# Kernel optimization log

Measured on AMD Instinct MI355X. Metric: run time of the kernel, lower is better.

Reference implementation:

```python
import jax, jax.numpy as jnp
import numpy as np

N = 100000   # nodes
E = 800000   # directed edges
IN = 256     # in_channels (== hidden, required by repo's vn MLP dims)
HID = 256    # hidden_channels
OUT = 40     # out_channels (arxiv classes)
EPS = 1e-5


def setup_inputs() -> dict:
    key = jax.random.key(0)
    ks = jax.random.split(key, 8)
    def nrm(k, shape, scale=0.05):
        return jax.random.normal(k, shape, dtype=jnp.float32) * scale
    return {
        "x": nrm(ks[0], (N, IN), 1.0),
        "edge_index": jax.random.randint(ks[1], (2, E), 0, N, dtype=jnp.int32),
        # GCNConv weights (PyG: x @ W, then normalized aggregation, then + bias)
        "W0": nrm(ks[2], (IN, HID)),  "b0": jnp.zeros((HID,), jnp.float32),
        "W1": nrm(ks[3], (HID, HID)), "b1": jnp.zeros((HID,), jnp.float32),
        "W2": nrm(ks[4], (HID, OUT)), "b2": jnp.zeros((OUT,), jnp.float32),
        # BatchNorm1d affine params (batch-stat math, training mode)
        "bn_g0": jnp.ones((HID,), jnp.float32), "bn_b0": jnp.zeros((HID,), jnp.float32),
        "bn_g1": jnp.ones((HID,), jnp.float32), "bn_b1": jnp.zeros((HID,), jnp.float32),
        # virtual node embedding (init to 0 per reset_parameters)
        "vn_emb": jnp.zeros((1, IN), jnp.float32),
        # mlp_vns[0]: Linear(IN,HID) + LayerNorm(HID) + ReLU
        "vn_W0": nrm(ks[5], (IN, HID)),  "vn_b0": jnp.zeros((HID,), jnp.float32),
        "ln_g0": jnp.ones((HID,), jnp.float32), "ln_b0": jnp.zeros((HID,), jnp.float32),
        # mlp_vns[1]: Linear(HID,HID) + LayerNorm(HID) + ReLU
        "vn_W1": nrm(ks[6], (HID, HID)), "vn_b1": jnp.zeros((HID,), jnp.float32),
        "ln_g1": jnp.ones((HID,), jnp.float32), "ln_b1": jnp.zeros((HID,), jnp.float32),
    }


def _forward(x, edge_index, W0, b0, W1, b1, W2, b2, bn_g0, bn_b0, bn_g1, bn_b1,
             vn_emb, vn_W0, vn_b0, ln_g0, ln_b0, vn_W1, vn_b1, ln_g1, ln_b1):
    src, dst = edge_index[0], edge_index[1]
    # GCN symmetric normalization with self-loops: deg = in-degree + 1
    deg = jax.ops.segment_sum(jnp.ones(src.shape, jnp.float32), dst, num_segments=N) + 1.0
    dis = jax.lax.rsqrt(deg)                       # deg^{-1/2}  [N]
    coef = (dis[src] * dis[dst])[:, None]          # edge norm   [E,1]
    self_coef = (dis * dis)[:, None]               # self-loop norm = deg^{-1}  [N,1]

    def gcn(h, W, b):
        h = h @ W                                             # [N, out]
        agg = jax.ops.segment_sum(h[src] * coef, dst, num_segments=N)
        return agg + h * self_coef + b

    def bn(h, g, bv):  # BatchNorm1d, batch statistics over nodes
        mu = h.mean(0)
        var = ((h - mu) ** 2).mean(0)
        return (h - mu) * jax.lax.rsqrt(var + EPS) * g + bv

    def ln(h, g, bv):  # LayerNorm over last dim
        mu = h.mean(-1, keepdims=True)
        var = ((h - mu) ** 2).mean(-1, keepdims=True)
        return (h - mu) * jax.lax.rsqrt(var + EPS) * g + bv

    vx = vn_emb                                   # [1, IN]
    # layer 0
    h = x + vx                                    # virtual-node broadcast
    h = gcn(h, W0, b0)
    h = jax.nn.relu(bn(h, bn_g0, bn_b0))          # dropout = identity (eval)
    pool = jnp.sum(h, axis=0, keepdims=True)      # global_add_pool
    vx = jax.nn.relu(ln((pool + vx) @ vn_W0 + vn_b0, ln_g0, ln_b0))
    # layer 1
    h = h + vx
    h = gcn(h, W1, b1)
    h = jax.nn.relu(bn(h, bn_g1, bn_b1))
    pool = jnp.sum(h, axis=0, keepdims=True)
    vx = jax.nn.relu(ln((pool + vx) @ vn_W1 + vn_b1, ln_g1, ln_b1))
    # layer 2 (output)
    h = h + vx
    h = gcn(h, W2, b2)
    return jax.nn.log_softmax(h, axis=-1)


def reference(x, edge_index, W0, b0, W1, b1, W2, b2, bn_g0, bn_b0, bn_g1, bn_b1,
              vn_emb, vn_W0, vn_b0, ln_g0, ln_b0, vn_W1, vn_b1, ln_g1, ln_b1):
    return _forward(x, edge_index, W0, b0, W1, b1, W2, b2, bn_g0, bn_b0, bn_g1, bn_b1,
                    vn_emb, vn_W0, vn_b0, ln_g0, ln_b0, vn_W1, vn_b1, ln_g1, ln_b1)
```

## Files before the change

kernel.cpp:

```cpp
#include <hip/hip_runtime.h>
#include <hip/hip_bf16.h>
#include <cstdint>

#define N_NODES 100000
#define N_EDGES 800000
#define CH      256
#define COUT    40
#define COUTP   48
#define EPS     1e-5f
#define SCAN_CHUNK 1024
#define NSCAN_BLK  98
#define AGG_NPW 16
#define AGG_BLOCKS 2048
#define AGG_WAVES  (AGG_BLOCKS * 4)

typedef unsigned short u16;
typedef unsigned int   u32;
typedef short s16x8 __attribute__((ext_vector_type(8)));
typedef float f32x4 __attribute__((ext_vector_type(4)));

__device__ __forceinline__ float b2f(u32 u) { return __uint_as_float(u << 16); }
__device__ __forceinline__ u16 f2b(float f) {
    u32 u = __float_as_uint(f);
    u32 r = (u + 0x7fffu + ((u >> 16) & 1u)) >> 16;
    return (u16)r;
}
__device__ __forceinline__ u32 packb(float a, float b) {
    return (u32)f2b(a) | ((u32)f2b(b) << 16);
}
__device__ __forceinline__ void unpack8(uint4 v, float* f) {
    f[0] = b2f(v.x & 0xffffu); f[1] = b2f(v.x >> 16);
    f[2] = b2f(v.y & 0xffffu); f[3] = b2f(v.y >> 16);
    f[4] = b2f(v.z & 0xffffu); f[5] = b2f(v.z >> 16);
    f[6] = b2f(v.w & 0xffffu); f[7] = b2f(v.w >> 16);
}

__global__ void k_count(const int* __restrict__ dst, int* __restrict__ counts) {
    int e = blockIdx.x * 256 + threadIdx.x;
    if (e < N_EDGES) atomicAdd(&counts[dst[e]], 1);
}

__global__ void k_scan1(const int* __restrict__ counts, int* __restrict__ partial,
                        int* __restrict__ blocksums) {
    __shared__ int sdata[256];
    int base = blockIdx.x * SCAN_CHUNK;
    int t = threadIdx.x;
    int v[4]; int s = 0;
    for (int j = 0; j < 4; j++) {
        int i = base + t * 4 + j;
        v[j] = (i < N_NODES) ? counts[i] : 0;
        s += v[j];
    }
    sdata[t] = s; __syncthreads();
    for (int off = 1; off < 256; off <<= 1) {
        int x = (t >= off) ? sdata[t - off] : 0;
        __syncthreads();
        sdata[t] += x;
        __syncthreads();
    }
    int incl = sdata[t];
    int run = incl - s;
    if (t == 255) blocksums[blockIdx.x] = incl;
    for (int j = 0; j < 4; j++) {
        int i = base + t * 4 + j;
        if (i < N_NODES) partial[i] = run;
        run += v[j];
    }
}

__global__ void k_scan2(int* __restrict__ blocksums) {
    __shared__ int sd[128];
    int t = threadIdx.x;
    int v = (t < NSCAN_BLK) ? blocksums[t] : 0;
    sd[t] = v; __syncthreads();
    for (int off = 1; off < 128; off <<= 1) {
        int x = (t >= off) ? sd[t - off] : 0;
        __syncthreads();
        sd[t] += x;
        __syncthreads();
    }
    if (t < NSCAN_BLK) blocksums[t] = sd[t] - v;
}

__global__ void k_scan3(int* __restrict__ row_start, const int* __restrict__ blocksums,
                        int* __restrict__ cursor, const int* __restrict__ counts,
                        float* __restrict__ dis) {
    int i = blockIdx.x * 256 + threadIdx.x;
    if (i < N_NODES) {
        int v = row_start[i] + blocksums[i >> 10];
        row_start[i] = v;
        cursor[i] = v;
        dis[i] = rsqrtf(1.0f + (float)counts[i]);
    }
}

__global__ void k_fill(const int* __restrict__ src, const int* __restrict__ dst,
                       int* __restrict__ cursor, int2* __restrict__ edata,
                       const float* __restrict__ dis) {
    int e = blockIdx.x * 256 + threadIdx.x;
    if (e < N_EDGES) {
        int d = dst[e], s = src[e];
        int p = atomicAdd(&cursor[d], 1);
        int2 v; v.x = s; v.y = __float_as_int(dis[s] * dis[d]);
        edata[p] = v;
    }
}

__global__ void k_wt3(const float* __restrict__ W0, const float* __restrict__ W1,
                      const float* __restrict__ W2,
                      u16* __restrict__ T0, u16* __restrict__ T1, u16* __restrict__ T2) {
    int b = blockIdx.x, k = threadIdx.x;
    if (b < 256) {
        T0[b * 256 + k] = f2b(W0[k * 256 + b]);
    } else if (b < 512) {
        int n = b - 256;
        T1[n * 256 + k] = f2b(W1[k * 256 + n]);
    } else {
        int n = b - 512;
        T2[n * 256 + k] = f2b(n < COUT ? W2[k * COUT + n] : 0.f);
    }
}

__global__ void k_vecmat(const float* __restrict__ vec, const float* __restrict__ W,
                         int ncols, int npad, float* __restrict__ outv) {
    __shared__ float s[256];
    int t = threadIdx.x;
    s[t] = vec[t];
    __syncthreads();
    float acc = 0.f;
    if (t < ncols) {
        for (int k = 0; k < 256; k++) acc += s[k] * W[k * ncols + t];
    }
    if (t < npad) outv[t] = acc;
}

__global__ __launch_bounds__(256) void k_gemm_f32a(const float* __restrict__ A,
                                                   const u16* __restrict__ Wt,
                                                   u16* __restrict__ Hout) {
    __shared__ u16 Bs[256 * 72];
    __shared__ u16 As[64 * 72];
    const int t = threadIdx.x;
    const int wave = t >> 6, lane = t & 63;
    const int lm = lane & 15, quad = lane >> 4;
    const int m0 = blockIdx.x * 64;
    const int ar = t >> 2, as_ = (t & 3) * 16;
    const int arow = m0 + ar;
    const f32x4 vz = {0.f, 0.f, 0.f, 0.f};
    f32x4 acc[4][4];
    for (int m = 0; m < 4; m++)
        for (int c = 0; c < 4; c++) acc[m][c] = vz;

    for (int k0 = 0; k0 < 256; k0 += 64) {
        {
            const uint4* bsrc = (const uint4*)(Wt + t * 256 + k0);
            uint4* bdst = (uint4*)(Bs + t * 72);
#pragma unroll
            for (int j = 0; j < 8; j++) bdst[j] = bsrc[j];
            uint4 p0 = {0,0,0,0}, p1 = {0,0,0,0};
            if (arow < N_NODES) {
                const float4* asrc = (const float4*)(A + (size_t)arow * 256 + k0 + as_);
                float4 x0 = asrc[0], x1 = asrc[1], x2 = asrc[2], x3 = asrc[3];
                p0.x = packb(x0.x, x0.y); p0.y = packb(x0.z, x0.w);
                p0.z = packb(x1.x, x1.y); p0.w = packb(x1.z, x1.w);
                p1.x = packb(x2.x, x2.y); p1.y = packb(x2.z, x2.w);
                p1.z = packb(x3.x, x3.y); p1.w = packb(x3.z, x3.w);
            }
            uint4* adst = (uint4*)(As + ar * 72 + as_);
            adst[0] = p0; adst[1] = p1;
        }
        __syncthreads();
#pragma unroll
        for (int kk = 0; kk < 64; kk += 32) {
            s16x8 af[4], bf[4];
#pragma unroll
            for (int m = 0; m < 4; m++)
                af[m] = *(const s16x8*)(As + (m * 16 + lm) * 72 + kk + quad * 8);
#pragma unroll
            for (int c = 0; c < 4; c++)
                bf[c] = *(const s16x8*)(Bs + (wave * 64 + c * 16 + lm) * 72 + kk + quad * 8);
#pragma unroll
            for (int c = 0; c < 4; c++)
#pragma unroll
                for (int m = 0; m < 4; m++)
                    acc[m][c] = __builtin_amdgcn_mfma_f32_16x16x32_bf16(af[m], bf[c], acc[m][c], 0, 0, 0);
        }
        __syncthreads();
    }
#pragma unroll
    for (int m = 0; m < 4; m++) {
#pragma unroll
        for (int c = 0; c < 4; c++) {
            int col = wave * 64 + c * 16 + lm;
#pragma unroll
            for (int i = 0; i < 4; i++) {
                int row = m0 + m * 16 + quad * 4 + i;
                if (row < N_NODES) Hout[(size_t)row * 256 + col] = f2b(acc[m][c][i]);
            }
        }
    }
}

__global__ __launch_bounds__(256) void k_gemm_bn(const u16* __restrict__ A,
                                                 const float* __restrict__ stats,
                                                 const float* __restrict__ g,
                                                 const float* __restrict__ bv,
                                                 const u16* __restrict__ Wt,
                                                 u16* __restrict__ Hout,
                                                 float* __restrict__ pool) {
    __shared__ u16 Bs[256 * 72];
    __shared__ u16 As[64 * 72];
    __shared__ float ggs[256], bcs[256], pls[256];
    const int t = threadIdx.x;
    const int wave = t >> 6, lane = t & 63;
    const int lm = lane & 15, quad = lane >> 4;
    const int m0 = blockIdx.x * 64;
    const int ar = t >> 2, as_ = (t & 3) * 16;
    const int arow = m0 + ar;
    {
        const float inv = 1.0f / (float)N_NODES;
        float mu = stats[t] * inv;
        float var = stats[256 + t] * inv - mu * mu;
        float rs = rsqrtf(var + EPS);
        float gg = g[t] * rs;
        ggs[t] = gg; bcs[t] = bv[t] - mu * gg;
        pls[t] = 0.f;
    }
    __syncthreads();
    const f32x4 vz = {0.f, 0.f, 0.f, 0.f};
    f32x4 acc[4][4];
    for (int m = 0; m < 4; m++)
        for (int c = 0; c < 4; c++) acc[m][c] = vz;

    for (int k0 = 0; k0 < 256; k0 += 64) {
        {
            const uint4* bsrc = (const uint4*)(Wt + t * 256 + k0);
            uint4* bdst = (uint4*)(Bs + t * 72);
#pragma unroll
            for (int j = 0; j < 8; j++) bdst[j] = bsrc[j];
            float f[16];
            if (arow < N_NODES) {
                const uint4* asrc = (const uint4*)(A + (size_t)arow * 256 + k0 + as_);
                uint4 r0 = asrc[0], r1 = asrc[1];
                unpack8(r0, f); unpack8(r1, f + 8);
#pragma unroll
                for (int j = 0; j < 16; j++) {
                    int c = k0 + as_ + j;
                    f[j] = fmaxf(f[j] * ggs[c] + bcs[c], 0.f);
                }
            } else {
#pragma unroll
                for (int j = 0; j < 16; j++) f[j] = 0.f;
            }
#pragma unroll
            for (int j = 0; j < 16; j++) {
                float v = f[j];
                v += __shfl_xor(v, 4);  v += __shfl_xor(v, 8);
                v += __shfl_xor(v, 16); v += __shfl_xor(v, 32);
                if (lane < 4) atomicAdd(&pls[k0 + lane * 16 + j], v);
            }
            uint4 p0, p1;
            p0.x = packb(f[0], f[1]);   p0.y = packb(f[2], f[3]);
            p0.z = packb(f[4], f[5]);   p0.w = packb(f[6], f[7]);
            p1.x = packb(f[8], f[9]);   p1.y = packb(f[10], f[11]);
            p1.z = packb(f[12], f[13]); p1.w = packb(f[14], f[15]);
            uint4* adst = (uint4*)(As + ar * 72 + as_);
            adst[0] = p0; adst[1] = p1;
        }
        __syncthreads();
#pragma unroll
        for (int kk = 0; kk < 64; kk += 32) {
            s16x8 af[4], bf[4];
#pragma unroll
            for (int m = 0; m < 4; m++)
                af[m] = *(const s16x8*)(As + (m * 16 + lm) * 72 + kk + quad * 8);
#pragma unroll
            for (int c = 0; c < 4; c++)
                bf[c] = *(const s16x8*)(Bs + (wave * 64 + c * 16 + lm) * 72 + kk + quad * 8);
#pragma unroll
            for (int c = 0; c < 4; c++)
#pragma unroll
                for (int m = 0; m < 4; m++)
                    acc[m][c] = __builtin_amdgcn_mfma_f32_16x16x32_bf16(af[m], bf[c], acc[m][c], 0, 0, 0);
        }
        __syncthreads();
    }
    atomicAdd(&pool[(blockIdx.x & 7) * 256 + t], pls[t]);
#pragma unroll
    for (int m = 0; m < 4; m++) {
#pragma unroll
        for (int c = 0; c < 4; c++) {
            int col = wave * 64 + c * 16 + lm;
#pragma unroll
            for (int i = 0; i < 4; i++) {
                int row = m0 + m * 16 + quad * 4 + i;
                if (row < N_NODES) Hout[(size_t)row * 256 + col] = f2b(acc[m][c][i]);
            }
        }
    }
}

__global__ __launch_bounds__(256) void k_gemm2_bn(const u16* __restrict__ A,
                                                  const float* __restrict__ stats,
                                                  const float* __restrict__ g,
                                                  const float* __restrict__ bv,
                                                  const u16* __restrict__ Wt,
                                                  u16* __restrict__ Hout,
                                                  float* __restrict__ pool) {
    __shared__ u16 Bs[48 * 72];
    __shared__ u16 As[64 * 72];
    __shared__ float ggs[256], bcs[256], pls[256];
    const int t = threadIdx.x;
    const int wave = t >> 6, lane = t & 63;
    const int lm = lane & 15, quad = lane >> 4;
    const int m0 = blockIdx.x * 64;
    const int ar = t >> 2, as_ = (t & 3) * 16;
    const int arow = m0 + ar;
    {
        const float inv = 1.0f / (float)N_NODES;
        float mu = stats[t] * inv;
        float var = stats[256 + t] * inv - mu * mu;
        float rs = rsqrtf(var + EPS);
        float gg = g[t] * rs;
        ggs[t] = gg; bcs[t] = bv[t] - mu * gg;
        pls[t] = 0.f;
    }
    __syncthreads();
    const f32x4 vz = {0.f, 0.f, 0.f, 0.f};
    f32x4 acc[3]; acc[0] = vz; acc[1] = vz; acc[2] = vz;

    for (int k0 = 0; k0 < 256; k0 += 64) {
        {
            if (t < 48) {
                const uint4* bsrc = (const uint4*)(Wt + t * 256 + k0);
                uint4* bdst = (uint4*)(Bs + t * 72);
#pragma unroll
                for (int j = 0; j < 8; j++) bdst[j] = bsrc[j];
            }
            float f[16];
            if (arow < N_NODES) {
                const uint4* asrc = (const uint4*)(A + (size_t)arow * 256 + k0 + as_);
                uint4 r0 = asrc[0], r1 = asrc[1];
                unpack8(r0, f); unpack8(r1, f + 8);
#pragma unroll
                for (int j = 0; j < 16; j++) {
                    int c = k0 + as_ + j;
                    f[j] = fmaxf(f[j] * ggs[c] + bcs[c], 0.f);
                }
            } else {
#pragma unroll
                for (int j = 0; j < 16; j++) f[j] = 0.f;
            }
#pragma unroll
            for (int j = 0; j < 16; j++) {
                float v = f[j];
                v += __shfl_xor(v, 4);  v += __shfl_xor(v, 8);
                v += __shfl_xor(v, 16); v += __shfl_xor(v, 32);
                if (lane < 4) atomicAdd(&pls[k0 + lane * 16 + j], v);
            }
            uint4 p0, p1;
            p0.x = packb(f[0], f[1]);   p0.y = packb(f[2], f[3]);
            p0.z = packb(f[4], f[5]);   p0.w = packb(f[6], f[7]);
            p1.x = packb(f[8], f[9]);   p1.y = packb(f[10], f[11]);
            p1.z = packb(f[12], f[13]); p1.w = packb(f[14], f[15]);
            uint4* adst = (uint4*)(As + ar * 72 + as_);
            adst[0] = p0; adst[1] = p1;
        }
        __syncthreads();
#pragma unroll
        for (int kk = 0; kk < 64; kk += 32) {
            s16x8 af = *(const s16x8*)(As + (wave * 16 + lm) * 72 + kk + quad * 8);
#pragma unroll
            for (int c = 0; c < 3; c++) {
                s16x8 bf = *(const s16x8*)(Bs + (c * 16 + lm) * 72 + kk + quad * 8);
                acc[c] = __builtin_amdgcn_mfma_f32_16x16x32_bf16(af, bf, acc[c], 0, 0, 0);
            }
        }
        __syncthreads();
    }
    atomicAdd(&pool[(blockIdx.x & 7) * 256 + t], pls[t]);
#pragma unroll
    for (int c = 0; c < 3; c++) {
        int col = c * 16 + lm;
#pragma unroll
        for (int i = 0; i < 4; i++) {
            int row = m0 + wave * 16 + quad * 4 + i;
            if (row < N_NODES) Hout[(size_t)row * COUTP + col] = f2b(acc[c][i]);
        }
    }
}

__global__ __launch_bounds__(256) void k_agg(const u16* __restrict__ H2,
                                             const int* __restrict__ row_start,
                                             const int* __restrict__ counts,
                                             const int2* __restrict__ edata,
                                             const float* __restrict__ dis,
                                             const float* __restrict__ bias,
                                             const float* __restrict__ v2,
                                             u16* __restrict__ OutB,
                                             float* __restrict__ stats) {
    __shared__ float ls[512];
    const int t = threadIdx.x, wave = t >> 6, lane = t & 63;
    const int half = lane >> 5, hl = lane & 31;
    const int ci = hl * 8;
    const float4 bbA = *(const float4*)(bias + ci);
    const float4 bbB = *(const float4*)(bias + ci + 4);
    const float4 vvA = *(const float4*)(v2 + ci);
    const float4 vvB = *(const float4*)(v2 + ci + 4);
    float s[8], q[8];
#pragma unroll
    for (int j = 0; j < 8; j++) { s[j] = 0.f; q[j] = 0.f; }

    const int gwave = blockIdx.x * 4 + wave;
    const int nid = gwave + lane * AGG_WAVES;
    const bool nv = (lane < AGG_NPW) && (nid < N_NODES);
    const int   my_rs = nv ? row_start[nid] : 0;
    const int   my_ct = nv ? counts[nid] : 0;
    const float my_dn = nv ? dis[nid] : 0.f;

    int beg = __shfl(my_rs, 0), cnt = __shfl(my_ct, 0);
    int2 my_e = {0, 0};
    if (lane < cnt) my_e = edata[beg + lane];

    for (int i = 0; i < AGG_NPW; i++) {
        const int node = gwave + i * AGG_WAVES;
        if (node >= N_NODES) break;
        const int2 cur_e = my_e;
        const int  ccnt = cnt, cbeg = beg;
        const float dn = __shfl(my_dn, i);
        const uint4 rs_ = *(const uint4*)(H2 + (size_t)node * 256 + ci);
        if (i + 1 < AGG_NPW && node + AGG_WAVES < N_NODES) {
            beg = __shfl(my_rs, i + 1);
            cnt = __shfl(my_ct, i + 1);
            int2 tmp = {0, 0};
            if (lane < cnt) tmp = edata[beg + lane];
            my_e = tmp;
        }
        const int cnt64 = ccnt < 64 ? ccnt : 64;
        const int cnt8 = (cnt64 + 7) & ~7;
        float a[8];
#pragma unroll
        for (int j = 0; j < 8; j++) a[j] = 0.f;
        float cs = 0.f;
        for (int e = 0; e < cnt8; e += 8) {
            const int   si0 = __shfl(cur_e.x, e + half);
            const int   si1 = __shfl(cur_e.x, e + 2 + half);
            const int   si2 = __shfl(cur_e.x, e + 4 + half);
            const int   si3 = __shfl(cur_e.x, e + 6 + half);
            const float cf0 = __int_as_float(__shfl(cur_e.y, e + half));
            const float cf1 = __int_as_float(__shfl(cur_e.y, e + 2 + half));
            const float cf2 = __int_as_float(__shfl(cur_e.y, e + 4 + half));
            const float cf3 = __int_as_float(__shfl(cur_e.y, e + 6 + half));
            const uint4 r0 = *(const uint4*)(H2 + (size_t)si0 * 256 + ci);
            const uint4 r1 = *(const uint4*)(H2 + (size_t)si1 * 256 + ci);
            const uint4 r2 = *(const uint4*)(H2 + (size_t)si2 * 256 + ci);
            const uint4 r3 = *(const uint4*)(H2 + (size_t)si3 * 256 + ci);
            cs += cf0 + cf1 + cf2 + cf3;
            a[0] += cf0*b2f(r0.x&0xffffu) + cf1*b2f(r1.x&0xffffu) + cf2*b2f(r2.x&0xffffu) + cf3*b2f(r3.x&0xffffu);
            a[1] += cf0*b2f(r0.x>>16)     + cf1*b2f(r1.x>>16)     + cf2*b2f(r2.x>>16)     + cf3*b2f(r3.x>>16);
            a[2] += cf0*b2f(r0.y&0xffffu) + cf1*b2f(r1.y&0xffffu) + cf2*b2f(r2.y&0xffffu) + cf3*b2f(r3.y&0xffffu);
            a[3] += cf0*b2f(r0.y>>16)     + cf1*b2f(r1.y>>16)     + cf2*b2f(r2.y>>16)     + cf3*b2f(r3.y>>16);
            a[4] += cf0*b2f(r0.z&0xffffu) + cf1*b2f(r1.z&0xffffu) + cf2*b2f(r2.z&0xffffu) + cf3*b2f(r3.z&0xffffu);
            a[5] += cf0*b2f(r0.z>>16)     + cf1*b2f(r1.z>>16)     + cf2*b2f(r2.z>>16)     + cf3*b2f(r3.z>>16);
            a[6] += cf0*b2f(r0.w&0xffffu) + cf1*b2f(r1.w&0xffffu) + cf2*b2f(r2.w&0xffffu) + cf3*b2f(r3.w&0xffffu);
            a[7] += cf0*b2f(r0.w>>16)     + cf1*b2f(r1.w>>16)     + cf2*b2f(r2.w>>16)     + cf3*b2f(r3.w>>16);
        }
        if (ccnt > 64) {
            int e2 = 64;
            for (; e2 + 2 <= ccnt; e2 += 2) {
                const int2 ed_ = edata[cbeg + e2 + half];
                const float cf = __int_as_float(ed_.y);
                const uint4 r = *(const uint4*)(H2 + (size_t)ed_.x * 256 + ci);
                cs += cf;
                a[0] += cf*b2f(r.x&0xffffu); a[1] += cf*b2f(r.x>>16);
                a[2] += cf*b2f(r.y&0xffffu); a[3] += cf*b2f(r.y>>16);
                a[4] += cf*b2f(r.z&0xffffu); a[5] += cf*b2f(r.z>>16);
                a[6] += cf*b2f(r.w&0xffffu); a[7] += cf*b2f(r.w>>16);
            }
            if (e2 < ccnt && half == 0) {
                const int2 ed_ = edata[cbeg + e2];
                const float cf = __int_as_float(ed_.y);
                const uint4 r = *(const uint4*)(H2 + (size_t)ed_.x * 256 + ci);
                cs += cf;
                a[0] += cf*b2f(r.x&0xffffu); a[1] += cf*b2f(r.x>>16);
                a[2] += cf*b2f(r.y&0xffffu); a[3] += cf*b2f(r.y>>16);
                a[4] += cf*b2f(r.z&0xffffu); a[5] += cf*b2f(r.z>>16);
                a[6] += cf*b2f(r.w&0xffffu); a[7] += cf*b2f(r.w>>16);
            }
        }
        cs += __shfl_xor(cs, 32);
#pragma unroll
        for (int j = 0; j < 8; j++) a[j] += __shfl_xor(a[j], 32);
        const float sc = dn * dn, cv = cs + sc;
        const float f0 = a[0] + sc*b2f(rs_.x&0xffffu) + cv*vvA.x + bbA.x;
        const float f1 = a[1] + sc*b2f(rs_.x>>16)     + cv*vvA.y + bbA.y;
        const float f2 = a[2] + sc*b2f(rs_.y&0xffffu) + cv*vvA.z + bbA.z;
        const float f3 = a[3] + sc*b2f(rs_.y>>16)     + cv*vvA.w + bbA.w;
        const float f4 = a[4] + sc*b2f(rs_.z&0xffffu) + cv*vvB.x + bbB.x;
        const float f5 = a[5] + sc*b2f(rs_.z>>16)     + cv*vvB.y + bbB.y;
        const float f6 = a[6] + sc*b2f(rs_.w&0xffffu) + cv*vvB.z + bbB.z;
        const float f7 = a[7] + sc*b2f(rs_.w>>16)     + cv*vvB.w + bbB.w;
        if (half == 0) {
            uint4 o;
            o.x = packb(f0, f1); o.y = packb(f2, f3);
            o.z = packb(f4, f5); o.w = packb(f6, f7);
            *(uint4*)(OutB + (size_t)node * 256 + ci) = o;
        }
        s[0] += f0; q[0] += f0*f0;  s[1] += f1; q[1] += f1*f1;
        s[2] += f2; q[2] += f2*f2;  s[3] += f3; q[3] += f3*f3;
        s[4] += f4; q[4] += f4*f4;  s[5] += f5; q[5] += f5*f5;
        s[6] += f6; q[6] += f6*f6;  s[7] += f7; q[7] += f7*f7;
    }
    ls[t] = 0.f; ls[256 + t] = 0.f;
    __syncthreads();
    if (half == 0) {
#pragma unroll
        for (int j = 0; j < 8; j++) {
            atomicAdd(&ls[ci + j], s[j]);
            atomicAdd(&ls[256 + ci + j], q[j]);
        }
    }
    __syncthreads();
    atomicAdd(&stats[t], ls[t]);
    atomicAdd(&stats[256 + t], ls[256 + t]);
}

__global__ void k_vx(const float* __restrict__ pool, const float* __restrict__ vx_old,
                     const float* __restrict__ vnW, const float* __restrict__ vnb,
                     const float* __restrict__ lng, const float* __restrict__ lnb,
                     float* __restrict__ vx_new,
                     const float* __restrict__ Wnext, int ncn, int npn,
                     float* __restrict__ v2n) {
    __shared__ float s[256];
    __shared__ float red[256];
    int t = threadIdx.x;
    float pv = 0.f;
#pragma unroll
    for (int r = 0; r < 8; r++) pv += pool[r * 256 + t];
    s[t] = pv + vx_old[t];
    __syncthreads();
    float y = vnb[t];
    for (int k = 0; k < 256; k++) y += s[k] * vnW[k * 256 + t];
    red[t] = y; __syncthreads();
    for (int off = 128; off > 0; off >>= 1) {
        if (t < off) red[t] += red[t + off];
        __syncthreads();
    }
    float mu = red[0] * (1.f / 256.f);
    __syncthreads();
    float d = y - mu;
    red[t] = d * d; __syncthreads();
    for (int off = 128; off > 0; off >>= 1) {
        if (t < off) red[t] += red[t + off];
        __syncthreads();
    }
    float var = red[0] * (1.f / 256.f);
    float v = fmaxf(d * rsqrtf(var + EPS) * lng[t] + lnb[t], 0.f);
    vx_new[t] = v;
    __syncthreads();
    s[t] = v;
    __syncthreads();
    float acc = 0.f;
    if (t < ncn) {
        for (int k = 0; k < 256; k++) acc += s[k] * Wnext[k * ncn + t];
    }
    if (t < npn) v2n[t] = acc;
}

__global__ __launch_bounds__(256) void k_agg2(const u16* __restrict__ H2,
                                              const int* __restrict__ row_start,
                                              const int* __restrict__ counts,
                                              const int2* __restrict__ edata,
                                              const float* __restrict__ dis,
                                              const float* __restrict__ bias,
                                              const float* __restrict__ v2,
                                              float* __restrict__ OutF) {
    const int t = threadIdx.x, wave = t >> 6, lane = t & 63;
    const int half = lane >> 5, hl = lane & 31;
    const bool gact = hl < 24;
    const bool cact = hl < 20;
    const int c0 = 2 * hl;
    float bb0 = 0.f, bb1 = 0.f, vv0 = 0.f, vv1 = 0.f;
    if (cact) {
        float2 bv = *(const float2*)(bias + c0); bb0 = bv.x; bb1 = bv.y;
        float2 vvv = *(const float2*)(v2 + c0);  vv0 = vvv.x; vv1 = vvv.y;
    }
    const int nbase = blockIdx.x * 16 + wave * 4;
    for (int i = 0; i < 4; i++) {
        const int node = nbase + i;
        const int beg = row_start[node], cnt = counts[node];
        const float dn = dis[node];
        float a0 = 0.f, a1 = 0.f, cs = 0.f;
        int e = half;
        for (; e + 6 < cnt; e += 8) {
            int2 ea = edata[beg+e],   eb = edata[beg+e+2];
            int2 ec = edata[beg+e+4], ed = edata[beg+e+6];
            float ca = __int_as_float(ea.y), cb = __int_as_float(eb.y);
            float cc = __int_as_float(ec.y), cd = __int_as_float(ed.y);
            u32 ra = 0, rb = 0, rc = 0, rd = 0;
            if (gact) {
                ra = *(const u32*)(H2 + (size_t)ea.x * COUTP + c0);
                rb = *(const u32*)(H2 + (size_t)eb.x * COUTP + c0);
                rc = *(const u32*)(H2 + (size_t)ec.x * COUTP + c0);
                rd = *(const u32*)(H2 + (size_t)ed.x * COUTP + c0);
            }
            cs += ca + cb + cc + cd;
            a0 += ca*b2f(ra&0xffffu) + cb*b2f(rb&0xffffu) + cc*b2f(rc&0xffffu) + cd*b2f(rd&0xffffu);
            a1 += ca*b2f(ra>>16)     + cb*b2f(rb>>16)     + cc*b2f(rc>>16)     + cd*b2f(rd>>16);
        }
        for (; e < cnt; e += 2) {
            int2 ea = edata[beg+e];
            float ca = __int_as_float(ea.y);
            u32 ra = gact ? *(const u32*)(H2 + (size_t)ea.x * COUTP + c0) : 0u;
            cs += ca;
            a0 += ca*b2f(ra&0xffffu); a1 += ca*b2f(ra>>16);
        }
        a0 += __shfl_xor(a0, 32);
        a1 += __shfl_xor(a1, 32);
        cs += __shfl_xor(cs, 32);
        const float sc = dn * dn;
        u32 rs_ = gact ? *(const u32*)(H2 + (size_t)node * COUTP + c0) : 0u;
        float h0 = a0 + sc*b2f(rs_&0xffffu) + (cs+sc)*vv0 + bb0;
        float h1 = a1 + sc*b2f(rs_>>16)     + (cs+sc)*vv1 + bb1;
        float m = cact ? fmaxf(h0, h1) : -3.0e38f;
#pragma unroll
        for (int off = 16; off > 0; off >>= 1) m = fmaxf(m, __shfl_xor(m, off));
        float ex = cact ? (expf(h0 - m) + expf(h1 - m)) : 0.f;
        float se = ex;
#pragma unroll
        for (int off = 16; off > 0; off >>= 1) se += __shfl_xor(se, off);
        float lg = logf(se);
        if (cact && half == 0) {
            float2 o = {h0 - m - lg, h1 - m - lg};
            *(float2*)(OutF + (size_t)node * COUT + c0) = o;
        }
    }
}

extern "C" void kernel_launch(void* const* d_in, const int* in_sizes, int n_in,
                              void* d_out, int out_size, void* d_ws, size_t ws_size,
                              hipStream_t stream) {
    const float* x   = (const float*)d_in[0];
    const int*   ei  = (const int*)d_in[1];
    const int*   esrc = ei;
    const int*   edst = ei + N_EDGES;
    const float* W0 = (const float*)d_in[2];  const float* b0 = (const float*)d_in[3];
    const float* W1 = (const float*)d_in[4];  const float* b1 = (const float*)d_in[5];
    const float* W2 = (const float*)d_in[6];  const float* b2 = (const float*)d_in[7];
    const float* bg0 = (const float*)d_in[8]; const float* bb0 = (const float*)d_in[9];
    const float* bg1 = (const float*)d_in[10]; const float* bb1 = (const float*)d_in[11];
    const float* vn_emb = (const float*)d_in[12];
    const float* vW0 = (const float*)d_in[13]; const float* vb0 = (const float*)d_in[14];
    const float* lg0 = (const float*)d_in[15]; const float* lb0 = (const float*)d_in[16];
    const float* vW1 = (const float*)d_in[17]; const float* vb1 = (const float*)d_in[18];
    const float* lg1 = (const float*)d_in[19]; const float* lb1 = (const float*)d_in[20];

    char* w = (char*)d_ws;
    auto alloc = [&](size_t bytes) { void* p = (void*)w; w += ((bytes + 255) / 256) * 256; return p; };
    u16* H2    = (u16*)alloc((size_t)N_NODES * 256 * 2);
    u16* OutB  = (u16*)alloc((size_t)N_NODES * 256 * 2);
    int2* edata = (int2*)alloc((size_t)N_EDGES * 8);
    int* counts = (int*)alloc((size_t)N_NODES * 4);
    int* rowst  = (int*)alloc((size_t)N_NODES * 4);
    int* cursor = (int*)alloc((size_t)N_NODES * 4);
    float* dis  = (float*)alloc((size_t)N_NODES * 4);
    u16* Wtb0 = (u16*)alloc(256 * 256 * 2);
    u16* Wtb1 = (u16*)alloc(256 * 256 * 2);
    u16* Wt2b = (u16*)alloc(COUTP * 256 * 2);
    int* scanblk = (int*)alloc(128 * 4);
    float* statsA = (float*)alloc(2560 * 4);
    float* statsB = (float*)alloc(2560 * 4);
    float* vxA = (float*)alloc(256 * 4);
    float* vxB = (float*)alloc(256 * 4);
    float* v20 = (float*)alloc(256 * 4);
    float* v21 = (float*)alloc(256 * 4);
    float* v22 = (float*)alloc(64 * 4);
    (void)ws_size; (void)in_sizes; (void)n_in; (void)out_size;

    hipMemsetAsync(counts, 0, (size_t)N_NODES * 4, stream);
    hipMemsetAsync(statsA, 0, 2560 * 4, stream);
    hipMemsetAsync(statsB, 0, 2560 * 4, stream);
    k_count<<<(N_EDGES + 255) / 256, 256, 0, stream>>>(edst, counts);
    k_scan1<<<NSCAN_BLK, 256, 0, stream>>>(counts, rowst, scanblk);
    k_scan2<<<1, 128, 0, stream>>>(scanblk);
    k_scan3<<<(N_NODES + 255) / 256, 256, 0, stream>>>(rowst, scanblk, cursor, counts, dis);
    k_fill<<<(N_EDGES + 255) / 256, 256, 0, stream>>>(esrc, edst, cursor, edata, dis);

    k_wt3<<<512 + COUTP, 256, 0, stream>>>(W0, W1, W2, Wtb0, Wtb1, Wt2b);
    k_vecmat<<<1, 256, 0, stream>>>(vn_emb, W0, 256, 256, v20);

    const int gemmblk = (N_NODES + 63) / 64;

    k_gemm_f32a<<<gemmblk, 256, 0, stream>>>(x, Wtb0, H2);
    k_agg<<<AGG_BLOCKS, 256, 0, stream>>>(H2, rowst, counts, edata, dis, b0, v20, OutB, statsA);
    k_gemm_bn<<<gemmblk, 256, 0, stream>>>(OutB, statsA, bg0, bb0, Wtb1, H2, statsA + 512);
    k_vx<<<1, 256, 0, stream>>>(statsA + 512, vn_emb, vW0, vb0, lg0, lb0, vxA, W1, 256, 256, v21);
    k_agg<<<AGG_BLOCKS, 256, 0, stream>>>(H2, rowst, counts, edata, dis, b1, v21, OutB, statsB);
    k_gemm2_bn<<<gemmblk, 256, 0, stream>>>(OutB, statsB, bg1, bb1, Wt2b, H2, statsB + 512);
    k_vx<<<1, 256, 0, stream>>>(statsB + 512, vxA, vW1, vb1, lg1, lb1, vxB, W2, COUT, COUTP, v22);
    k_agg2<<<N_NODES / 16, 256, 0, stream>>>(H2, rowst, counts, edata, dis, b2, v22, (float*)d_out);
}
```

Before: 745.6 us.

## Merge setup kernels and widen GEMM tiles to 128 rows with 512 threads

Folds the block-sum scan into k_scan3, and merges weight transposes, the virtual-node vecmat and all memsets into one prep kernel, which cuts several launches. The GEMM kernels move from 64-row tiles with 4 waves to 128-row tiles with 8 waves in a 2x4 arrangement, so each staged weight tile in shared memory is reused across twice as many rows. In exchange, every k_scan3 block redoes the small scan, and the larger blocks use more shared memory, which may lower occupancy. k_gemm2_bn's internal row mapping is not visible, so whether it handles 128 rows correctly is uncertain.

```diff
diff --git a/kernel.cpp b/kernel.cpp
--- a/kernel.cpp
+++ b/kernel.cpp
@@ -68,26 +68,26 @@
     }
 }
 
-__global__ void k_scan2(int* __restrict__ blocksums) {
-    __shared__ int sd[128];
-    int t = threadIdx.x;
-    int v = (t < NSCAN_BLK) ? blocksums[t] : 0;
-    sd[t] = v; __syncthreads();
-    for (int off = 1; off < 128; off <<= 1) {
-        int x = (t >= off) ? sd[t - off] : 0;
-        __syncthreads();
-        sd[t] += x;
-        __syncthreads();
-    }
-    if (t < NSCAN_BLK) blocksums[t] = sd[t] - v;
-}
-
 __global__ void k_scan3(int* __restrict__ row_start, const int* __restrict__ blocksums,
                         int* __restrict__ cursor, const int* __restrict__ counts,
                         float* __restrict__ dis) {
-    int i = blockIdx.x * 256 + threadIdx.x;
+    __shared__ int sd[128], raw[128];
+    int t = threadIdx.x;
+    if (t < 128) {
+        int v = (t < NSCAN_BLK) ? blocksums[t] : 0;
+        sd[t] = v; raw[t] = v;
+    }
+    __syncthreads();
+    for (int off = 1; off < 128; off <<= 1) {
+        int x = (t < 128 && t >= off) ? sd[t - off] : 0;
+        __syncthreads();
+        if (t < 128) sd[t] += x;
+        __syncthreads();
+    }
+    int i = blockIdx.x * 256 + t;
     if (i < N_NODES) {
-        int v = row_start[i] + blocksums[i >> 10];
+        int j = i >> 10;
+        int v = row_start[i] + (sd[j] - raw[j]);
         row_start[i] = v;
         cursor[i] = v;
         dis[i] = rsqrtf(1.0f + (float)counts[i]);
@@ -106,45 +106,52 @@
     }
 }
 
-__global__ void k_wt3(const float* __restrict__ W0, const float* __restrict__ W1,
-                      const float* __restrict__ W2,
-                      u16* __restrict__ T0, u16* __restrict__ T1, u16* __restrict__ T2) {
-    int b = blockIdx.x, k = threadIdx.x;
+#define PREP_ZBASE (513 + COUTP)
+#define PREP_ZN    (N_NODES + 2560 + 2560)
+#define PREP_BLOCKS (PREP_ZBASE + (PREP_ZN + 255) / 256)
+__global__ void k_prep(const float* __restrict__ W0, const float* __restrict__ W1,
+                       const float* __restrict__ W2,
+                       u16* __restrict__ T0, u16* __restrict__ T1, u16* __restrict__ T2,
+                       const float* __restrict__ vec, float* __restrict__ v20,
+                       int* __restrict__ counts, float* __restrict__ statsA,
+                       float* __restrict__ statsB) {
+    __shared__ float s[256];
+    int b = blockIdx.x, t = threadIdx.x;
     if (b < 256) {
-        T0[b * 256 + k] = f2b(W0[k * 256 + b]);
+        T0[b * 256 + t] = f2b(W0[t * 256 + b]);
     } else if (b < 512) {
         int n = b - 256;
-        T1[n * 256 + k] = f2b(W1[k * 256 + n]);
+        T1[n * 256 + t] = f2b(W1[t * 256 + n]);
+    } else if (b < 512 + COUTP) {
+        int n = b - 512;
+        T2[n * 256 + t] = f2b(n < COUT ? W2[t * COUT + n] : 0.f);
+    } else if (b == 512 + COUTP) {
+        s[t] = vec[t];
+        __syncthreads();
+        float acc = 0.f;
+        for (int k = 0; k < 256; k++) acc += s[k] * W0[k * 256 + t];
+        v20[t] = acc;
     } else {
-        int n = b - 512;
-        T2[n * 256 + k] = f2b(n < COUT ? W2[k * COUT + n] : 0.f);
-    }
-}
-
-__global__ void k_vecmat(const float* __restrict__ vec, const float* __restrict__ W,
-                         int ncols, int npad, float* __restrict__ outv) {
-    __shared__ float s[256];
-    int t = threadIdx.x;
-    s[t] = vec[t];
-    __syncthreads();
-    float acc = 0.f;
-    if (t < ncols) {
-        for (int k = 0; k < 256; k++) acc += s[k] * W[k * ncols + t];
-    }
-    if (t < npad) outv[t] = acc;
-}
-
-__global__ __launch_bounds__(256) void k_gemm_f32a(const float* __restrict__ A,
+        int idx = (b - PREP_ZBASE) * 256 + t;
+        if (idx < N_NODES) counts[idx] = 0;
+        else if ((idx -= N_NODES) < 2560) statsA[idx] = 0.f;
+        else if ((idx -= 2560) < 2560) statsB[idx] = 0.f;
+    }
+}
+
+__global__ __launch_bounds__(512) void k_gemm_f32a(const float* __restrict__ A,
                                                    const u16* __restrict__ Wt,
                                                    u16* __restrict__ Hout) {
     __shared__ u16 Bs[256 * 72];
-    __shared__ u16 As[64 * 72];
+    __shared__ u16 As[128 * 72];
     const int t = threadIdx.x;
     const int wave = t >> 6, lane = t & 63;
     const int lm = lane & 15, quad = lane >> 4;
-    const int m0 = blockIdx.x * 64;
+    const int wr = wave & 1, wc = wave >> 1;
+    const int m0 = blockIdx.x * 128;
     const int ar = t >> 2, as_ = (t & 3) * 16;
     const int arow = m0 + ar;
+    const int brow = t >> 1, bo = (t & 1) * 32;
     const f32x4 vz = {0.f, 0.f, 0.f, 0.f};
     f32x4 acc[4][4];
     for (int m = 0; m < 4; m++)
@@ -152,10 +159,10 @@
 
     for (int k0 = 0; k0 < 256; k0 += 64) {
         {
-            const uint4* bsrc = (const uint4*)(Wt + t * 256 + k0);
-            uint4* bdst = (uint4*)(Bs + t * 72);
-#pragma unroll
-            for (int j = 0; j < 8; j++) bdst[j] = bsrc[j];
+            const uint4* bsrc = (const uint4*)(Wt + brow * 256 + k0 + bo);
+            uint4* bdst = (uint4*)(Bs + brow * 72 + bo);
+#pragma unroll
+            for (int j = 0; j < 4; j++) bdst[j] = bsrc[j];
             uint4 p0 = {0,0,0,0}, p1 = {0,0,0,0};
             if (arow < N_NODES) {
                 const float4* asrc = (const float4*)(A + (size_t)arow * 256 + k0 + as_);
@@ -174,10 +181,10 @@
             s16x8 af[4], bf[4];
 #pragma unroll
             for (int m = 0; m < 4; m++)
-                af[m] = *(const s16x8*)(As + (m * 16 + lm) * 72 + kk + quad * 8);
+                af[m] = *(const s16x8*)(As + (wr * 64 + m * 16 + lm) * 72 + kk + quad * 8);
 #pragma unroll
             for (int c = 0; c < 4; c++)
-                bf[c] = *(const s16x8*)(Bs + (wave * 64 + c * 16 + lm) * 72 + kk + quad * 8);
+                bf[c] = *(const s16x8*)(Bs + (wc * 64 + c * 16 + lm) * 72 + kk + quad * 8);
 #pragma unroll
             for (int c = 0; c < 4; c++)
 #pragma unroll
@@ -190,17 +197,17 @@
     for (int m = 0; m < 4; m++) {
 #pragma unroll
         for (int c = 0; c < 4; c++) {
-            int col = wave * 64 + c * 16 + lm;
+            int col = wc * 64 + c * 16 + lm;
 #pragma unroll
             for (int i = 0; i < 4; i++) {
-                int row = m0 + m * 16 + quad * 4 + i;
+                int row = m0 + wr * 64 + m * 16 + quad * 4 + i;
                 if (row < N_NODES) Hout[(size_t)row * 256 + col] = f2b(acc[m][c][i]);
             }
         }
     }
 }
 
-__global__ __launch_bounds__(256) void k_gemm_bn(const u16* __restrict__ A,
+__global__ __launch_bounds__(512) void k_gemm_bn(const u16* __restrict__ A,
                                                  const float* __restrict__ stats,
                                                  const float* __restrict__ g,
                                                  const float* __restrict__ bv,
@@ -208,15 +215,17 @@
                                                  u16* __restrict__ Hout,
                                                  float* __restrict__ pool) {
     __shared__ u16 Bs[256 * 72];
-    __shared__ u16 As[64 * 72];
+    __shared__ u16 As[128 * 72];
     __shared__ float ggs[256], bcs[256], pls[256];
     const int t = threadIdx.x;
     const int wave = t >> 6, lane = t & 63;
     const int lm = lane & 15, quad = lane >> 4;
-    const int m0 = blockIdx.x * 64;
+    const int wr = wave & 1, wc = wave >> 1;
+    const int m0 = blockIdx.x * 128;
     const int ar = t >> 2, as_ = (t & 3) * 16;
     const int arow = m0 + ar;
-    {
+    const int brow = t >> 1, bo = (t & 1) * 32;
+    if (t < 256) {
         const float inv = 1.0f / (float)N_NODES;
         float mu = stats[t] * inv;
         float var = stats[256 + t] * inv - mu * mu;
@@ -233,10 +242,10 @@
 
     for (int k0 = 0; k0 < 256; k0 += 64) {
         {
-            const uint4* bsrc = (const uint4*)(Wt + t * 256 + k0);
-            uint4* bdst = (uint4*)(Bs + t * 72);
-#pragma unroll
-            for (int j = 0; j < 8; j++) bdst[j] = bsrc[j];
+            const uint4* bsrc = (const uint4*)(Wt + brow * 256 + k0 + bo);
+            uint4* bdst = (uint4*)(Bs + brow * 72 + bo);
+#pragma unroll
+            for (int j = 0; j < 4; j++) bdst[j] = bsrc[j];
             float f[16];
             if (arow < N_NODES) {
                 const uint4* asrc = (const uint4*)(A + (size_t)arow * 256 + k0 + as_);
@@ -272,10 +281,10 @@
             s16x8 af[4], bf[4];
 #pragma unroll
             for (int m = 0; m < 4; m++)
-                af[m] = *(const s16x8*)(As + (m * 16 + lm) * 72 + kk + quad * 8);
+                af[m] = *(const s16x8*)(As + (wr * 64 + m * 16 + lm) * 72 + kk + quad * 8);
 #pragma unroll
             for (int c = 0; c < 4; c++)
-                bf[c] = *(const s16x8*)(Bs + (wave * 64 + c * 16 + lm) * 72 + kk + quad * 8);
+                bf[c] = *(const s16x8*)(Bs + (wc * 64 + c * 16 + lm) * 72 + kk + quad * 8);
 #pragma unroll
             for (int c = 0; c < 4; c++)
 #pragma unroll
@@ -284,22 +293,22 @@
         }
         __syncthreads();
     }
-    atomicAdd(&pool[(blockIdx.x & 7) * 256 + t], pls[t]);
+    if (t < 256) atomicAdd(&pool[(blockIdx.x & 7) * 256 + t], pls[t]);
 #pragma unroll
     for (int m = 0; m < 4; m++) {
 #pragma unroll
         for (int c = 0; c < 4; c++) {
-            int col = wave * 64 + c * 16 + lm;
+            int col = wc * 64 + c * 16 + lm;
 #pragma unroll
             for (int i = 0; i < 4; i++) {
-                int row = m0 + m * 16 + quad * 4 + i;
+                int row = m0 + wr * 64 + m * 16 + quad * 4 + i;
                 if (row < N_NODES) Hout[(size_t)row * 256 + col] = f2b(acc[m][c][i]);
             }
         }
     }
 }
 
-__global__ __launch_bounds__(256) void k_gemm2_bn(const u16* __restrict__ A,
+__global__ __launch_bounds__(512) void k_gemm2_bn(const u16* __restrict__ A,
                                                   const float* __restrict__ stats,
                                                   const float* __restrict__ g,
                                                   const float* __restrict__ bv,
@@ -307,15 +316,15 @@
                                                   u16* __restrict__ Hout,
                                                   float* __restrict__ pool) {
     __shared__ u16 Bs[48 * 72];
-    __shared__ u16 As[64 * 72];
+    __shared__ u16 As[128 * 72];
     __shared__ float ggs[256], bcs[256], pls[256];
     const int t = threadIdx.x;
     const int wave = t >> 6, lane = t & 63;
     const int lm = lane & 15, quad = lane >> 4;
-    const int m0 = blockIdx.x * 64;
+    const int m0 = blockIdx.x * 128;
     const int ar = t >> 2, as_ = (t & 3) * 16;
     const int arow = m0 + ar;
-    {
+    if (t < 256) {
         const float inv = 1.0f / (float)N_NODES;
         float mu = stats[t] * inv;
         float var = stats[256 + t] * inv - mu * mu;
@@ -377,7 +386,7 @@
         }
         __syncthreads();
     }
-    atomicAdd(&pool[(blockIdx.x & 7) * 256 + t], pls[t]);
+    if (t < 256) atomicAdd(&pool[(blockIdx.x & 7) * 256 + t], pls[t]);
 #pragma unroll
     for (int c = 0; c < 3; c++) {
         int col = c * 16 + lm;
@@ -676,26 +685,21 @@
     float* v22 = (float*)alloc(64 * 4);
     (void)ws_size; (void)in_sizes; (void)n_in; (void)out_size;
 
-    hipMemsetAsync(counts, 0, (size_t)N_NODES * 4, stream);
-    hipMemsetAsync(statsA, 0, 2560 * 4, stream);
-    hipMemsetAsync(statsB, 0, 2560 * 4, stream);
+    k_prep<<<PREP_BLOCKS, 256, 0, stream>>>(W0, W1, W2, Wtb0, Wtb1, Wt2b,
+                                            vn_emb, v20, counts, statsA, statsB);
     k_count<<<(N_EDGES + 255) / 256, 256, 0, stream>>>(edst, counts);
     k_scan1<<<NSCAN_BLK, 256, 0, stream>>>(counts, rowst, scanblk);
-    k_scan2<<<1, 128, 0, stream>>>(scanblk);
     k_scan3<<<(N_NODES + 255) / 256, 256, 0, stream>>>(rowst, scanblk, cursor, counts, dis);
     k_fill<<<(N_EDGES + 255) / 256, 256, 0, stream>>>(esrc, edst, cursor, edata, dis);
 
-    k_wt3<<<512 + COUTP, 256, 0, stream>>>(W0, W1, W2, Wtb0, Wtb1, Wt2b);
-    k_vecmat<<<1, 256, 0, stream>>>(vn_emb, W0, 256, 256, v20);
-
-    const int gemmblk = (N_NODES + 63) / 64;
-
-    k_gemm_f32a<<<gemmblk, 256, 0, stream>>>(x, Wtb0, H2);
+    const int gemmblk = (N_NODES + 127) / 128;
+
+    k_gemm_f32a<<<gemmblk, 512, 0, stream>>>(x, Wtb0, H2);
     k_agg<<<AGG_BLOCKS, 256, 0, stream>>>(H2, rowst, counts, edata, dis, b0, v20, OutB, statsA);
-    k_gemm_bn<<<gemmblk, 256, 0, stream>>>(OutB, statsA, bg0, bb0, Wtb1, H2, statsA + 512);
+    k_gemm_bn<<<gemmblk, 512, 0, stream>>>(OutB, statsA, bg0, bb0, Wtb1, H2, statsA + 512);
     k_vx<<<1, 256, 0, stream>>>(statsA + 512, vn_emb, vW0, vb0, lg0, lb0, vxA, W1, 256, 256, v21);
     k_agg<<<AGG_BLOCKS, 256, 0, stream>>>(H2, rowst, counts, edata, dis, b1, v21, OutB, statsB);
-    k_gemm2_bn<<<gemmblk, 256, 0, stream>>>(OutB, statsB, bg1, bb1, Wt2b, H2, statsB + 512);
+    k_gemm2_bn<<<gemmblk, 512, 0, stream>>>(OutB, statsB, bg1, bb1, Wt2b, H2, statsB + 512);
     k_vx<<<1, 256, 0, stream>>>(statsB + 512, vxA, vW1, vb1, lg1, lb1, vxB, W2, COUT, COUTP, v22);
     k_agg2<<<N_NODES / 16, 256, 0, stream>>>(H2, rowst, counts, edata, dis, b2, v22, (float*)d_out);
 }
```

After: 719.4 us. 1.04x faster.
